# Kernel tuning notes

Measured on AMD Instinct MI355X. Metric: run time of the kernel, lower is better.

Reference implementation:

```python
import jax, jax.numpy as jnp
import numpy as np

B, T, S, K, L = 16, 32, 256, 8, 64
V, EXTRA, H, E = 32000, 50, 512, 512
VX = V + EXTRA
NEG = -1e10


def setup_inputs():
    key = jax.random.key(0)
    ks = jax.random.split(key, 40)
    f32 = jnp.float32

    def nrm(i, shape, scale=1.0):
        return (jax.random.normal(ks[i], shape) * scale).astype(f32)

    return {
        "tgt_input": jax.random.randint(ks[0], (B, T), 0, V),
        "initial_hidden": nrm(1, (1, B, H)),
        "src_outputs": nrm(2, (B, S, H)),
        "src_padding_mask": jnp.ones((B, 1, S), f32),
        "kg_hidden": nrm(3, (B, K, H)),
        "kg_fusion": nrm(4, (B, 1, H)),
        "kg_outputs": nrm(5, (B * K, L, H)),
        "kg_mask": jnp.ones((B, 1, K), f32),
        "kg_padding_mask": jnp.ones((B * K, 1, L), f32),
        "global_kg_dist": jax.random.uniform(ks[6], (B, 1, K), f32),
        "kg_extend_vocab": jax.random.randint(ks[7], (B, K, L), 0, VX),
        "extra_zero": jnp.zeros((B, 1, EXTRA), f32),
        # learned parameters (PyTorch Linear convention: y = x @ W.T + b)
        "embedding": nrm(8, (V, E), 0.05),
        "W_ih": nrm(9, (3 * H, E + 2 * H), 0.02),
        "W_hh": nrm(10, (3 * H, H), 0.02),
        "b_ih": jnp.zeros((3 * H,), f32),
        "b_hh": jnp.zeros((3 * H,), f32),
        "Wq_c": nrm(11, (H, H), 0.02),
        "Wv_c": nrm(12, (H, H), 0.02),
        "bv_c": jnp.zeros((H,), f32),
        "Vw_c": nrm(13, (1, H), 0.05),
        "bV_c": jnp.zeros((1,), f32),
        "Wq_k": nrm(14, (H, H), 0.02),
        "Wv_k": nrm(15, (H, H), 0.02),
        "bv_k": jnp.zeros((H,), f32),
        "Vw_k": nrm(16, (1, H), 0.05),
        "bV_k": jnp.zeros((1,), f32),
        "W1": nrm(17, (H, 4 * H), 0.02),
        "b1": jnp.zeros((H,), f32),
        "W2": nrm(18, (V, H), 0.02),
        "b2": jnp.zeros((V,), f32),
        "Wptr": nrm(19, (1, 4 * H + E), 0.02),
        "bptr": jnp.zeros((1,), f32),
        "Wcpy": nrm(20, (H, H), 0.02),
        "bcpy": jnp.zeros((H,), f32),
    }


def reference(tgt_input, initial_hidden, src_outputs, src_padding_mask, kg_hidden,
              kg_fusion, kg_outputs, kg_mask, kg_padding_mask, global_kg_dist,
              kg_extend_vocab, extra_zero, embedding, W_ih, W_hh, b_ih, b_hh,
              Wq_c, Wv_c, bv_c, Vw_c, bV_c, Wq_k, Wv_k, bv_k, Vw_k, bV_k,
              W1, b1, W2, b2, Wptr, bptr, Wcpy, bcpy):
    embed_tgt = embedding[tgt_input]                       # [B,T,E]
    h0 = initial_hidden[0]                                 # [B,H]
    kg_out4 = kg_outputs.reshape(B, K, L, H)
    # value projections of ConcatAttention are loop-invariant -> precompute
    pv_src = src_outputs @ Wv_c.T + bv_c                   # [B,S,H]
    pv_kg = kg_hidden @ Wv_k.T + bv_k                      # [B,K,H]
    src_bias = (src_padding_mask == 0.0) * NEG             # [B,1,S]
    kg_bias = (kg_mask == 0.0) * NEG                       # [B,1,K]
    copy_bias = (kg_padding_mask.reshape(B, K, L) == 0.0) * NEG
    kf = kg_fusion[:, 0]                                   # [B,H]
    ez = extra_zero[:, 0]                                  # [B,EXTRA]
    idx = kg_extend_vocab.reshape(B, K * L)

    def attend(hq, pv, value, bias, Wq, Vw, bV):
        # hq [B,H], pv/value [B,N,H], bias [B,1,N]
        t = jnp.tanh((hq @ Wq.T)[:, None, :] + pv)         # [B,N,H]
        e = t @ Vw[0] + bV[0]                              # [B,N]
        w = jax.nn.softmax(e[:, None, :] + bias, axis=-1)  # [B,1,N]
        return (w @ value)[:, 0], w[:, 0]

    def step(h, y_t):
        c_t, _ = attend(h, pv_src, src_outputs, src_bias, Wq_c, Vw_c, bV_c)
        k_t, k_w = attend(h, pv_kg, kg_hidden, kg_bias, Wq_k, Vw_k, bV_k)
        x = jnp.concatenate([y_t, c_t, k_t], axis=-1)
        gi = x @ W_ih.T + b_ih
        gh = h @ W_hh.T + b_hh
        i_r, i_z, i_n = jnp.split(gi, 3, axis=-1)
        h_r, h_z, h_n = jnp.split(gh, 3, axis=-1)
        r = jax.nn.sigmoid(i_r + h_r)
        z = jax.nn.sigmoid(i_z + h_z)
        n = jnp.tanh(i_n + r * h_n)
        s_t = (1.0 - z) * n + z * h                        # GRU output == new hidden
        ptr = jax.nn.sigmoid(
            jnp.concatenate([c_t, s_t, y_t, kf, k_t], axis=-1) @ Wptr.T + bptr)  # [B,1]
        q = s_t @ Wcpy.T + bcpy                            # [B,H]
        dist = jax.nn.softmax(
            jnp.einsum('bh,bklh->bkl', q, kg_out4) + copy_bias, axis=-1)  # [B,K,L]
        gen = jax.nn.softmax(
            (jnp.concatenate([s_t, c_t, k_t, kf], axis=-1) @ W1.T + b1) @ W2.T + b2,
            axis=-1) * ptr                                 # [B,V]
        fd = jnp.concatenate([gen, ez], axis=-1)           # [B,VX]
        # the torch loop of K scatter_adds == one scatter_add over K*L entries
        val = (dist * k_w[:, :, None] * (1.0 - ptr)[:, :, None]).reshape(B, K * L)
        fd = jax.vmap(lambda f, i_, v: f.at[i_].add(v))(fd, idx, val)
        fd = fd / fd.sum(axis=-1, keepdims=True)
        return s_t, fd

    _, outs = jax.lax.scan(step, h0, jnp.swapaxes(embed_tgt, 0, 1))  # [T,B,VX]
    return jnp.swapaxes(outs, 0, 1)                        # [B,T,VX]
```

## Files before the change

kernel.cpp:

```cpp
#include <hip/hip_runtime.h>
#include <hip/hip_bf16.h>

#define B_ 16
#define T_ 32
#define S_ 256
#define K_ 8
#define L_ 64
#define V_ 32000
#define VX_ 32050
#define NEG_ -1e10f
#define NBLK_ 128
#define BARSTRIDE_ 288

typedef __attribute__((ext_vector_type(8))) __bf16 bf16x8;
typedef __attribute__((ext_vector_type(8))) unsigned short us8;
typedef __attribute__((ext_vector_type(4))) float f32x4;

__device__ __forceinline__ float fsigmoid(float x){ return 1.f/(1.f+__expf(-x)); }
__device__ __forceinline__ float ftanh(float x){ float e=__expf(2.f*x); return 1.f - 2.f/(e+1.f); }
__device__ __forceinline__ unsigned short bf16rne(float f){
  unsigned u = __float_as_uint(f);
  u = u + 0x7FFFu + ((u >> 16) & 1u);
  return (unsigned short)(u >> 16);
}

__device__ __forceinline__ unsigned ld_llc_u32(const unsigned* p){
  unsigned v;
  asm volatile("global_load_dword %0, %1, off sc0 sc1\n\ts_waitcnt vmcnt(0)" : "=&v"(v) : "v"(p));
  return v;
}
__device__ __forceinline__ float ld_llc_f(const float* p){
  float v;
  asm volatile("global_load_dword %0, %1, off sc0 sc1\n\ts_waitcnt vmcnt(0)" : "=&v"(v) : "v"(p));
  return v;
}
__device__ __forceinline__ f32x4 ld_llc_f4(const float* p){
  f32x4 v;
  asm volatile("global_load_dwordx4 %0, %1, off sc0 sc1\n\ts_waitcnt vmcnt(0)" : "=&v"(v) : "v"(p));
  return v;
}
__device__ __forceinline__ void ld_llc_f4x2(const float* p, f32x4& a, f32x4& b){
  asm volatile("global_load_dwordx4 %0, %2, off sc0 sc1\n\t"
               "global_load_dwordx4 %1, %2, off offset:16 sc0 sc1\n\t"
               "s_waitcnt vmcnt(0)"
               : "=&v"(a), "=&v"(b) : "v"(p));
}
__device__ __forceinline__ void st_llc_f(float* p, float v){
  asm volatile("global_store_dword %0, %1, off sc0 sc1" :: "v"(p), "v"(v) : "memory");
}

__device__ __forceinline__ void pbar(unsigned* base, int blk){
  asm volatile("s_waitcnt vmcnt(0)" ::: "memory");
  __syncthreads();
  if (threadIdx.x == 0){
    unsigned* g = base + (blk & 7)*32;
    unsigned* root = base + 256;
    unsigned old = __hip_atomic_fetch_add(g, 1u, __ATOMIC_RELAXED, __HIP_MEMORY_SCOPE_AGENT);
    if (old == 15u)
      __hip_atomic_fetch_add(root, 1u, __ATOMIC_RELAXED, __HIP_MEMORY_SCOPE_AGENT);
    while (ld_llc_u32(root) < 8u) __builtin_amdgcn_s_sleep(1);
  }
  __syncthreads();
}

__global__ __launch_bounds__(256) void k_prep(const float* __restrict__ emb, const int* __restrict__ tgt,
    const float* __restrict__ src, const float* __restrict__ Wv_c, const float* __restrict__ bv_c,
    const float* __restrict__ kgh, const float* __restrict__ Wv_k, const float* __restrict__ bv_k,
    const float* __restrict__ W_ih,
    float* __restrict__ Xb, float* __restrict__ PVS, float* __restrict__ PVK, float* __restrict__ GIY){
  const int bid = blockIdx.x, tid = threadIdx.x;
  if (bid >= 360){
    int idx = (bid-360)*256 + tid;
    int t = idx >> 13; int b = (idx >> 9) & 15; int e = idx & 511;
    int tok = tgt[b*T_ + t];
    Xb[(size_t)(t*B_+b)*1536 + e] = emb[(size_t)tok*512 + e];
    return;
  }
  __shared__ float As[16][132];
  __shared__ float Ws[16][68];
  const float *A, *W, *bias; float* C; int ldA, ldW, ldC, m0, n0; bool gather = false;
  if (bid < 256){      A=src; ldA=512; W=Wv_c; ldW=512; bias=bv_c; C=PVS; ldC=512;
                       m0=(bid&31)*128; n0=(bid>>5)*64; }
  else if (bid < 264){ A=kgh; ldA=512; W=Wv_k; ldW=512; bias=bv_k; C=PVK; ldC=512;
                       m0=0; n0=(bid-256)*64; }
  else {               gather=true; A=nullptr; ldA=0; W=W_ih; ldW=1536; bias=nullptr; C=GIY; ldC=1536;
                       int g=bid-264; m0=(g&3)*128; n0=(g>>2)*64; }
  const int tm = tid & 15, tn = tid >> 4;
  float acc[8][4];
#pragma unroll
  for (int i=0;i<8;++i)
#pragma unroll
    for(int j=0;j<4;++j) acc[i][j]=0.f;
  for (int k0=0;k0<512;k0+=16){
#pragma unroll
    for (int rr=0;rr<2;++rr){
      int f = tid + rr*256;
      int mm = f >> 2, kc = f & 3;
      int m = m0 + mm;
      const float* ap;
      if (gather){
        int tok = tgt[(m & 15)*T_ + (m >> 4)];
        ap = emb + (size_t)tok*512 + k0 + kc*4;
      } else {
        ap = A + (size_t)m*ldA + k0 + kc*4;
      }
      const float4 v = *(const float4*)ap;
      As[kc*4+0][mm]=v.x; As[kc*4+1][mm]=v.y; As[kc*4+2][mm]=v.z; As[kc*4+3][mm]=v.w;
    }
    {
      int nn = tid >> 2, kc = tid & 3;
      const float4 v = *(const float4*)(W + (size_t)(n0+nn)*ldW + k0 + kc*4);
      Ws[kc*4+0][nn]=v.x; Ws[kc*4+1][nn]=v.y; Ws[kc*4+2][nn]=v.z; Ws[kc*4+3][nn]=v.w;
    }
    __syncthreads();
#pragma unroll
    for (int kk=0;kk<16;++kk){
      float a[8], w[4];
      float4 a0 = *(const float4*)&As[kk][tm*8];
      float4 a1 = *(const float4*)&As[kk][tm*8+4];
      float4 w0 = *(const float4*)&Ws[kk][tn*4];
      a[0]=a0.x;a[1]=a0.y;a[2]=a0.z;a[3]=a0.w;a[4]=a1.x;a[5]=a1.y;a[6]=a1.z;a[7]=a1.w;
      w[0]=w0.x;w[1]=w0.y;w[2]=w0.z;w[3]=w0.w;
#pragma unroll
      for (int i=0;i<8;++i)
#pragma unroll
        for (int j=0;j<4;++j) acc[i][j] += a[i]*w[j];
    }
    __syncthreads();
  }
#pragma unroll
  for (int i=0;i<8;++i){
    int m = m0 + tm*8 + i;
#pragma unroll
    for (int j=0;j<4;++j){
      int n = n0 + tn*4 + j;
      C[(size_t)m*ldC + n] = acc[i][j] + (bias ? bias[n] : 0.f);
    }
  }
}

struct RP4 {
  const float *inith, *src, *smask, *kgh, *kmask;
  const float *Wq_c, *Wq_k, *Vw_c, *bV_c, *Vw_k, *bV_k;
  const float *W_ih, *W_hh, *b_ih, *b_hh;
  const float *PVS, *PVK, *GIY;
  float *Xb, *S_all, *KW;
  float *HQC, *HQK, *GH, *CK, *Hbuf, *Eg;
  unsigned *cnt;
};

__global__ __launch_bounds__(512) void k_recur4(RP4 p){
  __shared__ float SH[4608];
  const int tid = threadIdx.x;
  const int blk = blockIdx.x;
  const float bVc = p.bV_c[0], bVk = p.bV_k[0];

  for (int t = 0; t < T_; ++t){
    {
      const int rg = blk & 31, bg = blk >> 5;
      float* hS = SH;
      {
        int i0 = tid*4; int bb = i0 >> 9, cc = i0 & 511;
        float vx,vy,vz,vw;
        if (t == 0){
          float4 v = *(const float4*)(p.inith + (size_t)(bg*4+bb)*512 + cc);
          vx=v.x; vy=v.y; vz=v.z; vw=v.w;
        } else {
          f32x4 v = ld_llc_f4(p.Hbuf + (size_t)(bg*4+bb)*512 + cc);
          vx=v[0]; vy=v[1]; vz=v[2]; vw=v[3];
        }
        hS[bb*516+cc]=vx; hS[bb*516+cc+1]=vy; hS[bb*516+cc+2]=vz; hS[bb*516+cc+3]=vw;
      }
      __syncthreads();
      int rl = tid >> 2, bl = tid & 3;
      if (rl < 80){
        int R = rg*80 + rl;
        const float* wrow = (R < 512) ? (p.Wq_c + (size_t)R*512)
                          : (R < 1024) ? (p.Wq_k + (size_t)(R-512)*512)
                          : (p.W_hh + (size_t)(R-1024)*512);
        const float* hb = hS + bl*516;
        float s = 0.f;
#pragma unroll 8
        for (int m=0;m<128;++m){
          float4 w = *(const float4*)(wrow + m*4);
          float4 hv = *(const float4*)(hb + m*4);
          s += w.x*hv.x + w.y*hv.y + w.z*hv.z + w.w*hv.w;
        }
        int b = bg*4 + bl;
        if (R < 512)       st_llc_f(p.HQC + b*512 + R, s);
        else if (R < 1024) st_llc_f(p.HQK + b*512 + (R-512), s);
        else               st_llc_f(p.GH + b*1536 + (R-1024), s + p.b_hh[R-1024]);
      }
    }
    pbar(p.cnt + (4*t)*BARSTRIDE_, blk);
    __syncthreads();

    {
      const int b2 = blk >> 3, pg = blk & 7;
      float* hqcS = SH;
      float* vwcS = SH + 528;
      {
        int q = tid >> 5, ii = tid & 31;
        if (tid < 512){
          hqcS[q*33+ii] = ld_llc_f(p.HQC + b2*512 + tid);
          vwcS[q*33+ii] = p.Vw_c[tid];
        }
      }
      __syncthreads();
      int pp = tid >> 4, q = tid & 15;
      int s_i = pg*32 + pp;
      const float4* pv4 = (const float4*)(p.PVS + ((size_t)(b2*S_ + s_i))*512 + q*32);
      const float* hq = hqcS + q*33;
      const float* vw = vwcS + q*33;
      float pe = 0.f;
#pragma unroll
      for (int m=0;m<8;++m){
        float4 v = pv4[m];
        int i0 = m*4;
        pe += ftanh(v.x+hq[i0+0])*vw[i0+0] + ftanh(v.y+hq[i0+1])*vw[i0+1]
            + ftanh(v.z+hq[i0+2])*vw[i0+2] + ftanh(v.w+hq[i0+3])*vw[i0+3];
      }
      pe += __shfl_down(pe, 8, 16);
      pe += __shfl_down(pe, 4, 16);
      pe += __shfl_down(pe, 2, 16);
      pe += __shfl_down(pe, 1, 16);
      if (q == 0){
        float v = pe + bVc;
        if (p.smask[b2*S_ + s_i] == 0.f) v += NEG_;
        st_llc_f(p.Eg + b2*S_ + s_i, v);
      }
    }
    pbar(p.cnt + (4*t+1)*BARSTRIDE_, blk);
    __syncthreads();

    {
      const int b3 = blk >> 3, jg = blk & 7, j0 = jg*64;
      float* eS    = SH;
      float* wS    = SH + 256;
      float* hqkS  = SH + 512;
      float* vwkS  = SH + 1088;
      float* partS = SH + 1664;
      float* ekS   = SH + 2176;
      float* kwS   = SH + 2184;
      float* MZ    = SH + 2192;
      if (tid < 64){
        f32x4 v = ld_llc_f4(p.Eg + b3*S_ + tid*4);
        eS[tid*4]=v[0]; eS[tid*4+1]=v[1]; eS[tid*4+2]=v[2]; eS[tid*4+3]=v[3];
      }
      {
        int part = tid >> 3, ii = tid & 7;
        hqkS[part*9+ii] = ld_llc_f(p.HQK + b3*512 + tid);
        vwkS[part*9+ii] = p.Vw_k[tid];
      }
      __syncthreads();
      if (tid < 64){
        float4 e4 = *(const float4*)&eS[tid*4];
        float m = fmaxf(fmaxf(e4.x,e4.y), fmaxf(e4.z,e4.w));
#pragma unroll
        for (int off=32; off>0; off>>=1) m = fmaxf(m, __shfl_xor(m, off, 64));
        float z = __expf(e4.x-m)+__expf(e4.y-m)+__expf(e4.z-m)+__expf(e4.w-m);
#pragma unroll
        for (int off=32; off>0; off>>=1) z += __shfl_xor(z, off, 64);
        if (tid == 0){ MZ[0] = m; MZ[1] = z; }
      }
      {
        int key = tid >> 6, part = tid & 63;
        const float4* pk4 = (const float4*)(p.PVK + ((size_t)(b3*K_ + key))*512 + part*8);
        float4 va = pk4[0], vb = pk4[1];
        const float* hq = hqkS + part*9;
        const float* vw = vwkS + part*9;
        float s2 = ftanh(va.x+hq[0])*vw[0] + ftanh(va.y+hq[1])*vw[1]
                 + ftanh(va.z+hq[2])*vw[2] + ftanh(va.w+hq[3])*vw[3]
                 + ftanh(vb.x+hq[4])*vw[4] + ftanh(vb.y+hq[5])*vw[5]
                 + ftanh(vb.z+hq[6])*vw[6] + ftanh(vb.w+hq[7])*vw[7];
#pragma unroll
        for (int off=32; off>0; off>>=1) s2 += __shfl_xor(s2, off, 64);
        if (part == 0){
          float v = s2 + bVk;
          if (p.kmask[b3*K_ + key] == 0.f) v += NEG_;
          ekS[key] = v;
        }
      }
      __syncthreads();
      if (tid == 0){
        float mk = -1e30f;
#pragma unroll
        for (int k=0;k<8;++k) mk = fmaxf(mk, ekS[k]);
        float z = 0.f; float tmp[8];
#pragma unroll
        for (int k=0;k<8;++k){ tmp[k] = __expf(ekS[k]-mk); z += tmp[k]; }
        float iz = 1.f/z;
#pragma unroll
        for (int k=0;k<8;++k) kwS[k] = tmp[k]*iz;
      }
      __syncthreads();
      float Mv = MZ[0], invZ = 1.f/MZ[1];
      if (tid < 256) wS[tid] = __expf(eS[tid]-Mv);
      __syncthreads();
      {
        int sg = tid >> 6, jl = tid & 63;
        const float* sp = p.src + ((size_t)(b3*S_ + sg*32))*512 + j0 + jl;
        float acc = 0.f;
#pragma unroll 8
        for (int i=0;i<32;++i) acc += wS[sg*32+i] * sp[(size_t)i*512];
        partS[sg*64 + jl] = acc;
      }
      __syncthreads();
      if (tid < 64){
        float c = 0.f;
#pragma unroll
        for (int sg=0; sg<8; ++sg) c += partS[sg*64 + tid];
        c *= invZ;
        float kt = 0.f;
#pragma unroll
        for (int k=0;k<8;++k) kt += kwS[k] * p.kgh[((size_t)(b3*K_+k))*512 + j0 + tid];
        float* Xbt = p.Xb + ((size_t)t*16 + b3)*1536;
        Xbt[512 + j0 + tid]  = c;
        Xbt[1024 + j0 + tid] = kt;
        st_llc_f(p.CK + b3*1024 + j0 + tid, c);
        st_llc_f(p.CK + b3*1024 + 512 + j0 + tid, kt);
      }
      if (jg == 0 && tid < 8) p.KW[t*128 + b3*8 + tid] = kwS[tid];
    }
    pbar(p.cnt + (4*t+2)*BARSTRIDE_, blk);
    __syncthreads();

    {
      const int rg2 = blk & 31, bg2 = blk >> 5;
      const int j0 = rg2*16, bb0 = bg2*4;
      float* ckS = SH;
      float* giS = SH + 4112;
      float* ghS = SH + 4304;
      {
        int i0 = tid*8; int bb = i0 >> 10, cc = i0 & 1023;
        f32x4 a, b4;
        ld_llc_f4x2(p.CK + (size_t)(bb0+bb)*1024 + cc, a, b4);
        float* d = ckS + bb*1028 + cc;
        d[0]=a[0]; d[1]=a[1]; d[2]=a[2]; d[3]=a[3];
        d[4]=b4[0]; d[5]=b4[1]; d[6]=b4[2]; d[7]=b4[3];
      }
      __syncthreads();
      int pair = tid >> 1, ks = tid & 1;
      float gi = 0.f;
      int row = 0, bloc = 0, rw = 0;
      if (pair < 192){
        rw = pair >> 2; bloc = pair & 3;
        row = (rw >> 4)*512 + j0 + (rw & 15);
        const float4* wi4 = (const float4*)(p.W_ih + (size_t)row*1536 + 512 + ks*512);
        const float* ckb = ckS + bloc*1028 + ks*512;
#pragma unroll 8
        for (int m=0;m<128;++m){
          float4 w = wi4[m];
          gi += w.x*ckb[m*4] + w.y*ckb[m*4+1] + w.z*ckb[m*4+2] + w.w*ckb[m*4+3];
        }
      }
      gi += __shfl_xor(gi, 1, 64);
      if (pair < 192 && ks == 0){
        int b = bb0 + bloc;
        giS[rw*4 + bloc] = gi + p.GIY[((size_t)t*16 + b)*1536 + row] + p.b_ih[row];
        ghS[rw*4 + bloc] = ld_llc_f(p.GH + b*1536 + row);
      }
      __syncthreads();
      if (tid < 64){
        int jl = tid >> 2, bl2 = tid & 3;
        int b = bb0 + bl2, j = j0 + jl;
        float gir = giS[jl*4+bl2],      giz = giS[(16+jl)*4+bl2],  gin = giS[(32+jl)*4+bl2];
        float ghr = ghS[jl*4+bl2],      ghz = ghS[(16+jl)*4+bl2],  ghn = ghS[(32+jl)*4+bl2];
        float r = fsigmoid(gir + ghr);
        float z = fsigmoid(giz + ghz);
        float n = ftanh(gin + r*ghn);
        float hold = (t == 0) ? p.inith[b*512 + j] : ld_llc_f(p.Hbuf + b*512 + j);
        float hn = (1.f - z)*n + z*hold;
        p.S_all[((size_t)t*16 + b)*512 + j] = hn;
        st_llc_f(p.Hbuf + b*512 + j, hn);
      }
    }
    pbar(p.cnt + (4*t+3)*BARSTRIDE_, blk);
    __syncthreads();
  }
}

__global__ __launch_bounds__(256) void k_epi(const float* __restrict__ S_all, const float* __restrict__ X,
    const float* __restrict__ kgf, const float* __restrict__ W1, const float* __restrict__ b1,
    const float* __restrict__ Wcpy, const float* __restrict__ bcpy,
    const float* __restrict__ Wptr, const float* __restrict__ bptr,
    float* __restrict__ HID, float* __restrict__ Qb, float* __restrict__ PTR){
  const int bid = blockIdx.x, tid = threadIdx.x;
  if (bid >= 64){
    int r = (bid-64)*4 + (tid >> 6);
    int lane = tid & 63;
    const float* seg[5];
    seg[0] = X + (size_t)r*1536 + 512;
    seg[1] = S_all + (size_t)r*512;
    seg[2] = X + (size_t)r*1536;
    seg[3] = kgf + (size_t)(r & 15)*512;
    seg[4] = X + (size_t)r*1536 + 1024;
    float s = 0.f;
#pragma unroll
    for (int g=0; g<5; ++g){
      const float* p = seg[g];
      const float* w = Wptr + g*512;
#pragma unroll
      for (int m=0;m<8;++m){ int i = lane + m*64; s += p[i]*w[i]; }
    }
#pragma unroll
    for (int off=32;off>0;off>>=1) s += __shfl_down(s, off, 64);
    if (lane == 0) PTR[r] = fsigmoid(s + bptr[0]);
    return;
  }
  __shared__ float As[16][132];
  __shared__ float Ws[16][68];
  const bool isW1 = (bid < 32);
  const int g = isW1 ? bid : bid-32;
  const int m0 = (g&3)*128, n0 = (g>>2)*64;
  const int KK = isW1 ? 2048 : 512;
  const float* W = isW1 ? W1 : Wcpy;
  const float* bias = isW1 ? b1 : bcpy;
  float* C = isW1 ? HID : Qb;
  const int tm = tid & 15, tn = tid >> 4;
  float acc[8][4];
#pragma unroll
  for (int i=0;i<8;++i)
#pragma unroll
    for(int j=0;j<4;++j) acc[i][j]=0.f;
  for (int k0=0;k0<KK;k0+=16){
#pragma unroll
    for (int rr=0;rr<2;++rr){
      int f = tid + rr*256;
      int mm = f >> 2, kc = f & 3;
      int m = m0 + mm, col = k0 + kc*4;
      const float* ap;
      if (!isW1)            ap = S_all + (size_t)m*512 + col;
      else if (col < 512)   ap = S_all + (size_t)m*512 + col;
      else if (col < 1536)  ap = X + (size_t)m*1536 + col;
      else                  ap = kgf + (size_t)(m & 15)*512 + (col - 1536);
      const float4 v = *(const float4*)ap;
      As[kc*4+0][mm]=v.x; As[kc*4+1][mm]=v.y; As[kc*4+2][mm]=v.z; As[kc*4+3][mm]=v.w;
    }
    {
      int nn = tid >> 2, kc = tid & 3;
      const float4 v = *(const float4*)(W + (size_t)(n0+nn)*KK + k0 + kc*4);
      Ws[kc*4+0][nn]=v.x; Ws[kc*4+1][nn]=v.y; Ws[kc*4+2][nn]=v.z; Ws[kc*4+3][nn]=v.w;
    }
    __syncthreads();
#pragma unroll
    for (int kk=0;kk<16;++kk){
      float a[8], w[4];
      float4 a0 = *(const float4*)&As[kk][tm*8];
      float4 a1 = *(const float4*)&As[kk][tm*8+4];
      float4 w0 = *(const float4*)&Ws[kk][tn*4];
      a[0]=a0.x;a[1]=a0.y;a[2]=a0.z;a[3]=a0.w;a[4]=a1.x;a[5]=a1.y;a[6]=a1.z;a[7]=a1.w;
      w[0]=w0.x;w[1]=w0.y;w[2]=w0.z;w[3]=w0.w;
#pragma unroll
      for (int i=0;i<8;++i)
#pragma unroll
        for (int j=0;j<4;++j) acc[i][j] += a[i]*w[j];
    }
    __syncthreads();
  }
#pragma unroll
  for (int i=0;i<8;++i){
    int m = m0 + tm*8 + i;
#pragma unroll
    for (int j=0;j<4;++j){
      int n = n0 + tn*4 + j;
      C[(size_t)m*512 + n] = acc[i][j] + bias[n];
    }
  }
}

__global__ __launch_bounds__(512) void k_logits(const float* __restrict__ A,
    const float* __restrict__ Bf, const float* __restrict__ bias, float* __restrict__ out){
  __shared__ unsigned short As[256][72];
  __shared__ unsigned short Bs[128][72];
  const int tid = threadIdx.x;
  const int m0 = blockIdx.x*256, n0 = blockIdx.y*128;
  const int lane = tid & 63, wid = tid >> 6;
  const int mw = wid >> 1, nw = wid & 1;
  f32x4 acc[4][4];
#pragma unroll
  for (int i=0;i<4;++i)
#pragma unroll
    for (int j=0;j<4;++j) acc[i][j] = (f32x4){0.f,0.f,0.f,0.f};
  for (int k0 = 0; k0 < 512; k0 += 64){
#pragma unroll
    for (int i=0;i<4;++i){
      int v = i*512 + tid; int row = v >> 3, vc = v & 7;
      const float* srcp = A + (size_t)(m0+row)*512 + k0 + vc*8;
      float4 f0 = *(const float4*)srcp, f1 = *(const float4*)(srcp+4);
      us8 d;
      d[0]=bf16rne(f0.x); d[1]=bf16rne(f0.y); d[2]=bf16rne(f0.z); d[3]=bf16rne(f0.w);
      d[4]=bf16rne(f1.x); d[5]=bf16rne(f1.y); d[6]=bf16rne(f1.z); d[7]=bf16rne(f1.w);
      *(us8*)&As[row][vc*8] = d;
    }
#pragma unroll
    for (int i=0;i<2;++i){
      int v = i*512 + tid; int row = v >> 3, vc = v & 7;
      const float* srcp = Bf + (size_t)(n0+row)*512 + k0 + vc*8;
      float4 f0 = *(const float4*)srcp, f1 = *(const float4*)(srcp+4);
      us8 d;
      d[0]=bf16rne(f0.x); d[1]=bf16rne(f0.y); d[2]=bf16rne(f0.z); d[3]=bf16rne(f0.w);
      d[4]=bf16rne(f1.x); d[5]=bf16rne(f1.y); d[6]=bf16rne(f1.z); d[7]=bf16rne(f1.w);
      *(us8*)&Bs[row][vc*8] = d;
    }
    __syncthreads();
#pragma unroll
    for (int kk=0;kk<2;++kk){
      bf16x8 a[4], bf[4];
#pragma unroll
      for (int mi=0;mi<4;++mi){
        int ar = mw*64 + mi*16 + (lane&15);
        a[mi] = *(const bf16x8*)&As[ar][(kk*4 + (lane>>4))*8];
      }
#pragma unroll
      for (int ni=0;ni<4;++ni){
        int br = nw*64 + ni*16 + (lane&15);
        bf[ni] = *(const bf16x8*)&Bs[br][(kk*4 + (lane>>4))*8];
      }
#pragma unroll
      for (int mi=0;mi<4;++mi)
#pragma unroll
        for (int ni=0;ni<4;++ni)
          acc[mi][ni] = __builtin_amdgcn_mfma_f32_16x16x32_bf16(a[mi], bf[ni], acc[mi][ni], 0, 0, 0);
    }
    __syncthreads();
  }
#pragma unroll
  for (int mi=0;mi<4;++mi){
#pragma unroll
    for (int r=0;r<4;++r){
      int gr = m0 + mw*64 + mi*16 + (lane>>4)*4 + r;
      size_t orow = (size_t)((gr&15)*32 + (gr>>4)) * VX_;
#pragma unroll
      for (int ni=0;ni<4;++ni){
        int col = n0 + nw*64 + ni*16 + (lane&15);
        out[orow + col] = acc[mi][ni][r] + bias[col];
      }
    }
  }
}

__global__ __launch_bounds__(256) void k_final(float* __restrict__ out, const float* __restrict__ PTR,
    const float* __restrict__ Q, const float* __restrict__ kgo, const float* __restrict__ kpmask,
    const int* __restrict__ kev, const float* __restrict__ KW){
  const int orow = blockIdx.x;
  const int b = orow >> 5, t = orow & 31;
  const int r = t*16 + b;
  const int tid = threadIdx.x;
  float* f = out + (size_t)orow * VX_;
  __shared__ float qs[512];
  __shared__ float part[256];
  __shared__ float red[256];
  __shared__ float valS[512];
  __shared__ int   idxS[512];
  const float ptr = PTR[r];
  qs[tid] = Q[(size_t)r*512 + tid];
  qs[256 + tid] = Q[(size_t)r*512 + 256 + tid];
  __syncthreads();
  for (int k = 0; k < 8; ++k){
    int l = tid >> 2, qtr = tid & 3;
    const float* kgrow = kgo + (size_t)((b*8 + k)*64 + l) * 512;
    float p = 0.f;
    const float4* q4 = (const float4*)(qs) + qtr*32;
    const float4* k4 = (const float4*)(kgrow) + qtr*32;
#pragma unroll 4
    for (int m=0;m<32;++m){ float4 a=q4[m], c=k4[m]; p += a.x*c.x+a.y*c.y+a.z*c.z+a.w*c.w; }
    part[tid] = p;
    __syncthreads();
    if (tid < 64){
      float ev = part[tid*4]+part[tid*4+1]+part[tid*4+2]+part[tid*4+3];
      if (kpmask[(b*8+k)*64 + tid] == 0.f) ev += NEG_;
      float mx = ev;
#pragma unroll
      for (int off=32;off>0;off>>=1) mx = fmaxf(mx, __shfl_xor(mx, off, 64));
      float ex = __expf(ev - mx);
      float z = ex;
#pragma unroll
      for (int off=32;off>0;off>>=1) z += __shfl_xor(z, off, 64);
      valS[k*64 + tid] = (ex/z) * KW[t*128 + b*8 + k] * (1.f - ptr);
      idxS[k*64 + tid] = kev[(b*8+k)*64 + tid];
    }
    __syncthreads();
  }
  float lm = -1e30f;
  for (int v = tid; v < V_; v += 256) lm = fmaxf(lm, f[v]);
  red[tid] = lm; __syncthreads();
  for (int s=128;s>0;s>>=1){ if (tid<s) red[tid]=fmaxf(red[tid],red[tid+s]); __syncthreads(); }
  float M = red[0]; __syncthreads();
  float ls = 0.f;
  for (int v = tid; v < V_; v += 256){ float e2 = __expf(f[v]-M); f[v] = e2; ls += e2; }
  red[tid] = ls; __syncthreads();
  for (int s=128;s>0;s>>=1){ if (tid<s) red[tid]+=red[tid+s]; __syncthreads(); }
  float scale = ptr / red[0];
  for (int v = tid; v < V_; v += 256) f[v] *= scale;
  for (int v = V_ + tid; v < VX_; v += 256) f[v] = 0.f;
  __syncthreads();
  atomicAdd(f + idxS[tid], valS[tid]);
  atomicAdd(f + idxS[256 + tid], valS[256 + tid]);
}

extern "C" void kernel_launch(void* const* d_in, const int* in_sizes, int n_in,
                              void* d_out, int out_size, void* d_ws, size_t ws_size,
                              hipStream_t stream) {
  const int*   tgt   = (const int*)  d_in[0];
  const float* inith = (const float*)d_in[1];
  const float* src   = (const float*)d_in[2];
  const float* smask = (const float*)d_in[3];
  const float* kgh   = (const float*)d_in[4];
  const float* kgf   = (const float*)d_in[5];
  const float* kgo   = (const float*)d_in[6];
  const float* kmask = (const float*)d_in[7];
  const float* kpmask= (const float*)d_in[8];
  const int*   kev   = (const int*)  d_in[10];
  const float* emb   = (const float*)d_in[12];
  const float* W_ih  = (const float*)d_in[13];
  const float* W_hh  = (const float*)d_in[14];
  const float* b_ih  = (const float*)d_in[15];
  const float* b_hh  = (const float*)d_in[16];
  const float* Wq_c  = (const float*)d_in[17];
  const float* Wv_c  = (const float*)d_in[18];
  const float* bv_c  = (const float*)d_in[19];
  const float* Vw_c  = (const float*)d_in[20];
  const float* bV_c  = (const float*)d_in[21];
  const float* Wq_k  = (const float*)d_in[22];
  const float* Wv_k  = (const float*)d_in[23];
  const float* bv_k  = (const float*)d_in[24];
  const float* Vw_k  = (const float*)d_in[25];
  const float* bV_k  = (const float*)d_in[26];
  const float* W1    = (const float*)d_in[27];
  const float* b1    = (const float*)d_in[28];
  const float* W2    = (const float*)d_in[29];
  const float* b2    = (const float*)d_in[30];
  const float* Wptr  = (const float*)d_in[31];
  const float* bptr  = (const float*)d_in[32];
  const float* Wcpy  = (const float*)d_in[33];
  const float* bcpy  = (const float*)d_in[34];
  float* out = (float*)d_out;

  float* Xb    = (float*)d_ws;
  float* S_all = Xb    + 786432;
  float* PVS   = S_all + 262144;
  float* PVK   = PVS   + 2097152;
  float* KW    = PVK   + 65536;
  float* GIY   = KW    + 4096;
  float* CK    = GIY   + 786432;
  float* HID   = CK    + 16384;
  float* Qb    = HID   + 262144;
  float* PTR   = Qb    + 262144;
  float* HQC   = PTR   + 512;
  float* HQK   = HQC   + 8192;
  float* GH    = HQK   + 8192;
  float* Hbuf  = GH    + 24576;
  float* Eg    = Hbuf  + 8192;
  unsigned* CNT = (unsigned*)(Eg + 4096);

  hipMemsetAsync(CNT, 0, 128*BARSTRIDE_*sizeof(unsigned), stream);

  k_prep<<<1384, 256, 0, stream>>>(emb, tgt, src, Wv_c, bv_c, kgh, Wv_k, bv_k, W_ih,
                                   Xb, PVS, PVK, GIY);

  RP4 rp { inith, src, smask, kgh, kmask, Wq_c, Wq_k, Vw_c, bV_c, Vw_k, bV_k,
           W_ih, W_hh, b_ih, b_hh, PVS, PVK, GIY, Xb, S_all, KW,
           HQC, HQK, GH, CK, Hbuf, Eg, CNT };
  k_recur4<<<NBLK_, 512, 0, stream>>>(rp);

  k_epi<<<192, 256, 0, stream>>>(S_all, Xb, kgf, W1, b1, Wcpy, bcpy, Wptr, bptr, HID, Qb, PTR);
  k_logits<<<dim3(2,250), 512, 0, stream>>>(HID, W2, b2, out);
  k_final<<<512, 256, 0, stream>>>(out, PTR, Qb, kgo, kpmask, kev, KW);
}
```

Measured before the change: 1.754 ms.

## Halve persistent recurrence grid to 64 blocks, doubling work per block per phase

The persistent GRU recurrence kernel now runs on 64 blocks instead of 128. Each of the four per-step phases is re-partitioned so a block covers twice as many rows, source positions and hidden columns, and the hierarchical grid barrier's group threshold is adjusted to match. The aim is to make each of the 128 grid barriers cheaper and to cut redundant per-block loads, at the cost of less parallelism and more serial work per block in every phase.

```diff
diff --git a/kernel.cpp b/kernel.cpp
--- a/kernel.cpp
+++ b/kernel.cpp
@@ -9,7 +9,7 @@
 #define V_ 32000
 #define VX_ 32050
 #define NEG_ -1e10f
-#define NBLK_ 128
+#define NBLK_ 64
 #define BARSTRIDE_ 288
 
 typedef __attribute__((ext_vector_type(8))) __bf16 bf16x8;
@@ -56,7 +56,7 @@
     unsigned* g = base + (blk & 7)*32;
     unsigned* root = base + 256;
     unsigned old = __hip_atomic_fetch_add(g, 1u, __ATOMIC_RELAXED, __HIP_MEMORY_SCOPE_AGENT);
-    if (old == 15u)
+    if (old == 7u)
       __hip_atomic_fetch_add(root, 1u, __ATOMIC_RELAXED, __HIP_MEMORY_SCOPE_AGENT);
     while (ld_llc_u32(root) < 8u) __builtin_amdgcn_s_sleep(1);
   }
@@ -139,7 +139,7 @@
   }
 }
 
-struct RP4 {
+struct RP7 {
   const float *inith, *src, *smask, *kgh, *kmask;
   const float *Wq_c, *Wq_k, *Vw_c, *bV_c, *Vw_k, *bV_k;
   const float *W_ih, *W_hh, *b_ih, *b_hh;
@@ -149,15 +149,15 @@
   unsigned *cnt;
 };
 
-__global__ __launch_bounds__(512) void k_recur4(RP4 p){
-  __shared__ float SH[4608];
+__global__ __launch_bounds__(512) void k_recur7(RP7 p){
+  __shared__ float SH[4992];
   const int tid = threadIdx.x;
   const int blk = blockIdx.x;
   const float bVc = p.bV_c[0], bVk = p.bV_k[0];
 
   for (int t = 0; t < T_; ++t){
     {
-      const int rg = blk & 31, bg = blk >> 5;
+      const int rg = blk & 15, bg = blk >> 4;
       float* hS = SH;
       {
         int i0 = tid*4; int bb = i0 >> 9, cc = i0 & 511;
@@ -173,57 +173,58 @@
       }
       __syncthreads();
       int rl = tid >> 2, bl = tid & 3;
-      if (rl < 80){
-        int R = rg*80 + rl;
-        const float* wrow = (R < 512) ? (p.Wq_c + (size_t)R*512)
-                          : (R < 1024) ? (p.Wq_k + (size_t)(R-512)*512)
-                          : (p.W_hh + (size_t)(R-1024)*512);
-        const float* hb = hS + bl*516;
-        float s = 0.f;
+      int b = bg*4 + bl;
+      const float* hb = hS + bl*516;
+#pragma unroll
+      for (int it = 0; it < 2; ++it){
+        int rr2 = rl + it*128;
+        if (rr2 < 160){
+          int R = rg*160 + rr2;
+          const float* wrow = (R < 512) ? (p.Wq_c + (size_t)R*512)
+                            : (R < 1024) ? (p.Wq_k + (size_t)(R-512)*512)
+                            : (p.W_hh + (size_t)(R-1024)*512);
+          float s = 0.f;
 #pragma unroll 8
-        for (int m=0;m<128;++m){
-          float4 w = *(const float4*)(wrow + m*4);
-          float4 hv = *(const float4*)(hb + m*4);
-          s += w.x*hv.x + w.y*hv.y + w.z*hv.z + w.w*hv.w;
+          for (int m=0;m<128;++m){
+            float4 w = *(const float4*)(wrow + m*4);
+            float4 hv = *(const float4*)(hb + m*4);
+            s += w.x*hv.x + w.y*hv.y + w.z*hv.z + w.w*hv.w;
+          }
+          if (R < 512)       st_llc_f(p.HQC + b*512 + R, s);
+          else if (R < 1024) st_llc_f(p.HQK + b*512 + (R-512), s);
+          else               st_llc_f(p.GH + b*1536 + (R-1024), s + p.b_hh[R-1024]);
         }
-        int b = bg*4 + bl;
-        if (R < 512)       st_llc_f(p.HQC + b*512 + R, s);
-        else if (R < 1024) st_llc_f(p.HQK + b*512 + (R-512), s);
-        else               st_llc_f(p.GH + b*1536 + (R-1024), s + p.b_hh[R-1024]);
       }
     }
     pbar(p.cnt + (4*t)*BARSTRIDE_, blk);
     __syncthreads();
 
     {
-      const int b2 = blk >> 3, pg = blk & 7;
+      const int b2 = blk >> 2, pg = blk & 3;
       float* hqcS = SH;
-      float* vwcS = SH + 528;
+      float* vwcS = SH + 520;
       {
-        int q = tid >> 5, ii = tid & 31;
-        if (tid < 512){
-          hqcS[q*33+ii] = ld_llc_f(p.HQC + b2*512 + tid);
-          vwcS[q*33+ii] = p.Vw_c[tid];
-        }
-      }
-      __syncthreads();
-      int pp = tid >> 4, q = tid & 15;
-      int s_i = pg*32 + pp;
-      const float4* pv4 = (const float4*)(p.PVS + ((size_t)(b2*S_ + s_i))*512 + q*32);
-      const float* hq = hqcS + q*33;
-      const float* vw = vwcS + q*33;
+        int chunk = tid >> 6, ii = tid & 63;
+        hqcS[chunk*65+ii] = ld_llc_f(p.HQC + b2*512 + tid);
+        vwcS[chunk*65+ii] = p.Vw_c[tid];
+      }
+      __syncthreads();
+      int pp = tid >> 3, q = tid & 7;
+      int s_i = pg*64 + pp;
+      const float4* pv4 = (const float4*)(p.PVS + ((size_t)(b2*S_ + s_i))*512 + q*64);
+      const float* hq = hqcS + q*65;
+      const float* vw = vwcS + q*65;
       float pe = 0.f;
 #pragma unroll
-      for (int m=0;m<8;++m){
+      for (int m=0;m<16;++m){
         float4 v = pv4[m];
         int i0 = m*4;
         pe += ftanh(v.x+hq[i0+0])*vw[i0+0] + ftanh(v.y+hq[i0+1])*vw[i0+1]
             + ftanh(v.z+hq[i0+2])*vw[i0+2] + ftanh(v.w+hq[i0+3])*vw[i0+3];
       }
-      pe += __shfl_down(pe, 8, 16);
-      pe += __shfl_down(pe, 4, 16);
-      pe += __shfl_down(pe, 2, 16);
-      pe += __shfl_down(pe, 1, 16);
+      pe += __shfl_down(pe, 4, 8);
+      pe += __shfl_down(pe, 2, 8);
+      pe += __shfl_down(pe, 1, 8);
       if (q == 0){
         float v = pe + bVc;
         if (p.smask[b2*S_ + s_i] == 0.f) v += NEG_;
@@ -234,7 +235,7 @@
     __syncthreads();
 
     {
-      const int b3 = blk >> 3, jg = blk & 7, j0 = jg*64;
+      const int b3 = blk >> 2, jg = blk & 3, j0 = jg*128;
       float* eS    = SH;
       float* wS    = SH + 256;
       float* hqkS  = SH + 512;
@@ -298,18 +299,16 @@
       if (tid < 256) wS[tid] = __expf(eS[tid]-Mv);
       __syncthreads();
       {
-        int sg = tid >> 6, jl = tid & 63;
-        const float* sp = p.src + ((size_t)(b3*S_ + sg*32))*512 + j0 + jl;
+        int sg = tid >> 7, jl = tid & 127;
+        const float* sp = p.src + ((size_t)(b3*S_ + sg*64))*512 + j0 + jl;
         float acc = 0.f;
 #pragma unroll 8
-        for (int i=0;i<32;++i) acc += wS[sg*32+i] * sp[(size_t)i*512];
-        partS[sg*64 + jl] = acc;
-      }
-      __syncthreads();
-      if (tid < 64){
-        float c = 0.f;
-#pragma unroll
-        for (int sg=0; sg<8; ++sg) c += partS[sg*64 + tid];
+        for (int i=0;i<64;++i) acc += wS[sg*64+i] * sp[(size_t)i*512];
+        partS[sg*128 + jl] = acc;
+      }
+      __syncthreads();
+      if (tid < 128){
+        float c = partS[tid] + partS[128 + tid] + partS[256 + tid] + partS[384 + tid];
         c *= invZ;
         float kt = 0.f;
 #pragma unroll
@@ -326,11 +325,11 @@
     __syncthreads();
 
     {
-      const int rg2 = blk & 31, bg2 = blk >> 5;
-      const int j0 = rg2*16, bb0 = bg2*4;
+      const int rg2 = blk & 15, bg2 = blk >> 4;
+      const int j0 = rg2*32, bb0 = bg2*4;
       float* ckS = SH;
       float* giS = SH + 4112;
-      float* ghS = SH + 4304;
+      float* ghS = SH + 4496;
       {
         int i0 = tid*8; int bb = i0 >> 10, cc = i0 & 1023;
         f32x4 a, b4;
@@ -341,31 +340,34 @@
       }
       __syncthreads();
       int pair = tid >> 1, ks = tid & 1;
-      float gi = 0.f;
-      int row = 0, bloc = 0, rw = 0;
-      if (pair < 192){
-        rw = pair >> 2; bloc = pair & 3;
-        row = (rw >> 4)*512 + j0 + (rw & 15);
-        const float4* wi4 = (const float4*)(p.W_ih + (size_t)row*1536 + 512 + ks*512);
-        const float* ckb = ckS + bloc*1028 + ks*512;
+#pragma unroll
+      for (int it = 0; it < 2; ++it){
+        int pr = pair + it*256;
+        if (pr < 384){
+          int rw = pr >> 2, bloc = pr & 3;
+          int row = (rw >> 5)*512 + j0 + (rw & 31);
+          const float4* wi4 = (const float4*)(p.W_ih + (size_t)row*1536 + 512 + ks*512);
+          const float* ckb = ckS + bloc*1028 + ks*512;
+          float gi = 0.f;
 #pragma unroll 8
-        for (int m=0;m<128;++m){
-          float4 w = wi4[m];
-          gi += w.x*ckb[m*4] + w.y*ckb[m*4+1] + w.z*ckb[m*4+2] + w.w*ckb[m*4+3];
+          for (int m=0;m<128;++m){
+            float4 w = wi4[m];
+            gi += w.x*ckb[m*4] + w.y*ckb[m*4+1] + w.z*ckb[m*4+2] + w.w*ckb[m*4+3];
+          }
+          gi += __shfl_xor(gi, 1, 64);
+          if (ks == 0){
+            int b = bb0 + bloc;
+            giS[rw*4 + bloc] = gi + p.GIY[((size_t)t*16 + b)*1536 + row] + p.b_ih[row];
+            ghS[rw*4 + bloc] = ld_llc_f(p.GH + b*1536 + row);
+          }
         }
       }
-      gi += __shfl_xor(gi, 1, 64);
-      if (pair < 192 && ks == 0){
-        int b = bb0 + bloc;
-        giS[rw*4 + bloc] = gi + p.GIY[((size_t)t*16 + b)*1536 + row] + p.b_ih[row];
-        ghS[rw*4 + bloc] = ld_llc_f(p.GH + b*1536 + row);
-      }
-      __syncthreads();
-      if (tid < 64){
+      __syncthreads();
+      if (tid < 128){
         int jl = tid >> 2, bl2 = tid & 3;
         int b = bb0 + bl2, j = j0 + jl;
-        float gir = giS[jl*4+bl2],      giz = giS[(16+jl)*4+bl2],  gin = giS[(32+jl)*4+bl2];
-        float ghr = ghS[jl*4+bl2],      ghz = ghS[(16+jl)*4+bl2],  ghn = ghS[(32+jl)*4+bl2];
+        float gir = giS[jl*4+bl2],      giz = giS[(32+jl)*4+bl2],  gin = giS[(64+jl)*4+bl2];
+        float ghr = ghS[jl*4+bl2],      ghz = ghS[(32+jl)*4+bl2],  ghn = ghS[(64+jl)*4+bl2];
         float r = fsigmoid(gir + ghr);
         float z = fsigmoid(giz + ghz);
         float n = ftanh(gin + r*ghn);
@@ -659,10 +661,10 @@
   k_prep<<<1384, 256, 0, stream>>>(emb, tgt, src, Wv_c, bv_c, kgh, Wv_k, bv_k, W_ih,
                                    Xb, PVS, PVK, GIY);
 
-  RP4 rp { inith, src, smask, kgh, kmask, Wq_c, Wq_k, Vw_c, bV_c, Vw_k, bV_k,
+  RP7 rp { inith, src, smask, kgh, kmask, Wq_c, Wq_k, Vw_c, bV_c, Vw_k, bV_k,
            W_ih, W_hh, b_ih, b_hh, PVS, PVK, GIY, Xb, S_all, KW,
            HQC, HQK, GH, CK, Hbuf, Eg, CNT };
-  k_recur4<<<NBLK_, 512, 0, stream>>>(rp);
+  k_recur7<<<NBLK_, 512, 0, stream>>>(rp);
 
   k_epi<<<192, 256, 0, stream>>>(S_all, Xb, kgf, W1, b1, Wcpy, bcpy, Wptr, bptr, HID, Qb, PTR);
   k_logits<<<dim3(2,250), 512, 0, stream>>>(HID, W2, b2, out);
```

Result: slower. 2.688 ms (+53.2%).
